# Performance work log

Hardware: AMD Instinct MI355X
Metric: run time of the kernel (lower is better)

## Reference

```python
import jax, jax.numpy as jnp
import numpy as np

N_P, N_A, D_MP = 200000, 100000, 64   # paper nodes, author nodes, metapath embed dim
E = 1200000                            # nnz per adjacency op
F_P, F_A = 256, 128                    # raw feature dims


def _spmm(row, col, val, z, n_out):
    # Sparse [n_out, n_in] @ dense [n_in, d]: out[i] = sum_{e: row[e]==i} val[e] * z[col[e]]
    return jax.ops.segment_sum(val[:, None] * z[col], row, num_segments=n_out)


def setup_inputs() -> dict:
    key = jax.random.key(0)
    k = jax.random.split(key, 10)
    return {
        "x_paper": jax.random.normal(k[0], (N_P, F_P), jnp.float32),
        "x_author": jax.random.normal(k[1], (N_A, F_A), jnp.float32),
        "W_paper": jax.random.normal(k[2], (F_P, D_MP), jnp.float32) / np.float32(np.sqrt(F_P)),
        "W_author": jax.random.normal(k[3], (F_A, D_MP), jnp.float32) / np.float32(np.sqrt(F_A)),
        "pa_row": jax.random.randint(k[4], (E,), 0, N_A, jnp.int32),
        "pa_col": jax.random.randint(k[5], (E,), 0, N_P, jnp.int32),
        "pa_val": jax.random.uniform(k[6], (E,), jnp.float32),
        "ap_row": jax.random.randint(k[7], (E,), 0, N_P, jnp.int32),
        "ap_col": jax.random.randint(k[8], (E,), 0, N_A, jnp.int32),
        "ap_val": jax.random.uniform(k[9], (E,), jnp.float32),
    }


def reference(x_paper, x_author, W_paper, W_author,
              pa_row, pa_col, pa_val, ap_row, ap_col, ap_val):
    # per-node-type projection (nn.Linear, no bias)
    zp = x_paper @ W_paper    # [N_P, D_MP]
    za = x_author @ W_author  # [N_A, D_MP]

    # metapath P-A-P: ops = [pa (N_A x N_P), ap (N_P x N_A)]
    h = _spmm(pa_row, pa_col, pa_val, zp, N_A)
    pap = _spmm(ap_row, ap_col, ap_val, h, N_P)

    # metapath P-A-P-A-P: 4 chained SpMMs
    h2 = _spmm(pa_row, pa_col, pa_val, pap, N_A)
    papap = _spmm(ap_row, ap_col, ap_val, h2, N_P)

    # metapath A-P-A: ops = [ap (N_P x N_A), pa (N_A x N_P)]
    g = _spmm(ap_row, ap_col, ap_val, za, N_P)
    apa = _spmm(pa_row, pa_col, pa_val, g, N_A)

    return (pap, papap, apa)
```

## Files before the change

kernel.cpp:

```cpp
#include <hip/hip_runtime.h>
#include <hip/hip_fp16.h>

#define NP 200000
#define NA 100000
#define NE 1200000


__global__ __launch_bounds__(256) void hist_k(const int* __restrict__ row, int* __restrict__ cnt, int n) {
    int i = blockIdx.x * blockDim.x + threadIdx.x;
    int stride = gridDim.x * blockDim.x;
    for (; i < n; i += stride) atomicAdd(&cnt[row[i]], 1);
}

__global__ __launch_bounds__(256) void scan1_k(const int* __restrict__ in, int* __restrict__ out,
                                               int* __restrict__ bsums, int n) {
    __shared__ int lds[256];
    int t = threadIdx.x;
    int base = blockIdx.x * 1024 + t * 4;
    int v0 = (base + 0 < n) ? in[base + 0] : 0;
    int v1 = (base + 1 < n) ? in[base + 1] : 0;
    int v2 = (base + 2 < n) ? in[base + 2] : 0;
    int v3 = (base + 3 < n) ? in[base + 3] : 0;
    lds[t] = v0 + v1 + v2 + v3;
    __syncthreads();
    for (int off = 1; off < 256; off <<= 1) {
        int x = (t >= off) ? lds[t - off] : 0;
        __syncthreads();
        lds[t] += x;
        __syncthreads();
    }
    if (t == 255) bsums[blockIdx.x] = lds[255];
    int run = (t == 0) ? 0 : lds[t - 1];
    if (base + 0 < n) out[base + 0] = run; run += v0;
    if (base + 1 < n) out[base + 1] = run; run += v1;
    if (base + 2 < n) out[base + 2] = run; run += v2;
    if (base + 3 < n) out[base + 3] = run;
}

__global__ void scan2_k(int* bsums, int nb) {
    __shared__ int lds[256];
    int t = threadIdx.x;
    int v = (t < nb) ? bsums[t] : 0;
    lds[t] = v;
    __syncthreads();
    for (int off = 1; off < 256; off <<= 1) {
        int x = (t >= off) ? lds[t - off] : 0;
        __syncthreads();
        lds[t] += x;
        __syncthreads();
    }
    if (t < nb) bsums[t] = (t == 0) ? 0 : lds[t - 1];
}

__global__ __launch_bounds__(256) void scan3_k(int* __restrict__ out, const int* __restrict__ bsums, int n) {
    int add = bsums[blockIdx.x];
    int base = blockIdx.x * 1024 + threadIdx.x * 4;
#pragma unroll
    for (int j = 0; j < 4; j++)
        if (base + j < n) out[base + j] += add;
}

__global__ __launch_bounds__(256) void scatter_k(const int* __restrict__ row, const int* __restrict__ col,
                                                 const float* __restrict__ val, const int* __restrict__ off,
                                                 int* __restrict__ cursor, int2* __restrict__ csr, int n) {
    int i = blockIdx.x * blockDim.x + threadIdx.x;
    int stride = gridDim.x * blockDim.x;
    for (; i < n; i += stride) {
        int r = row[i];
        int pos = off[r] + atomicAdd(&cursor[r], 1);
        csr[pos] = make_int2(col[i], __float_as_int(val[i]));
    }
}


__device__ __forceinline__ void fma_h8(float acc[8], float v, uint4 r) {
    __half2 h0 = *(__half2*)&r.x;
    __half2 h1 = *(__half2*)&r.y;
    __half2 h2 = *(__half2*)&r.z;
    __half2 h3 = *(__half2*)&r.w;
    float2 f0 = __half22float2(h0);
    float2 f1 = __half22float2(h1);
    float2 f2 = __half22float2(h2);
    float2 f3 = __half22float2(h3);
    acc[0] = fmaf(v, f0.x, acc[0]);
    acc[1] = fmaf(v, f0.y, acc[1]);
    acc[2] = fmaf(v, f1.x, acc[2]);
    acc[3] = fmaf(v, f1.y, acc[3]);
    acc[4] = fmaf(v, f2.x, acc[4]);
    acc[5] = fmaf(v, f2.y, acc[5]);
    acc[6] = fmaf(v, f3.x, acc[6]);
    acc[7] = fmaf(v, f3.y, acc[7]);
}

__device__ __forceinline__ void store_h8(uint4* out16, int g, int l, const float acc[8]) {
    __half2 p0 = __floats2half2_rn(acc[0], acc[1]);
    __half2 p1 = __floats2half2_rn(acc[2], acc[3]);
    __half2 p2 = __floats2half2_rn(acc[4], acc[5]);
    __half2 p3 = __floats2half2_rn(acc[6], acc[7]);
    uint4 o;
    o.x = *(unsigned*)&p0;
    o.y = *(unsigned*)&p1;
    o.z = *(unsigned*)&p2;
    o.w = *(unsigned*)&p3;
    out16[(size_t)g * 8 + l] = o;
}

__device__ __forceinline__ void store_f8(float4* out32, int g, int l, const float acc[8]) {
    out32[(size_t)g * 16 + l * 2 + 0] = make_float4(acc[0], acc[1], acc[2], acc[3]);
    out32[(size_t)g * 16 + l * 2 + 1] = make_float4(acc[4], acc[5], acc[6], acc[7]);
}

__global__ __launch_bounds__(256) void spmm_k(const int2* __restrict__ csr, const int* __restrict__ off,
                                              const int* __restrict__ cnt, const uint4* __restrict__ z,
                                              float4* __restrict__ out32, uint4* __restrict__ out16,
                                              int nrows) {
    int g = blockIdx.x * 32 + (threadIdx.x >> 3);
    int l = threadIdx.x & 7;
    if (g >= nrows) return;
    int start = off[g], deg = cnt[g];
    float acc[8];
#pragma unroll
    for (int i = 0; i < 8; i++) acc[i] = 0.f;
    for (int j = 0; j < deg; j += 4) {
        int j1 = min(j + 1, deg - 1);
        int j2 = min(j + 2, deg - 1);
        int j3 = min(j + 3, deg - 1);
        int2 e0 = csr[start + j];
        int2 e1 = csr[start + j1];
        int2 e2 = csr[start + j2];
        int2 e3 = csr[start + j3];
        uint4 r0 = z[e0.x * 8 + l];
        uint4 r1 = z[e1.x * 8 + l];
        uint4 r2 = z[e2.x * 8 + l];
        uint4 r3 = z[e3.x * 8 + l];
        float v0 = __int_as_float(e0.y);
        float v1 = (j + 1 < deg) ? __int_as_float(e1.y) : 0.f;
        float v2 = (j + 2 < deg) ? __int_as_float(e2.y) : 0.f;
        float v3 = (j + 3 < deg) ? __int_as_float(e3.y) : 0.f;
        fma_h8(acc, v0, r0);
        fma_h8(acc, v1, r1);
        fma_h8(acc, v2, r2);
        fma_h8(acc, v3, r3);
    }
    if (out32) store_f8(out32, g, l, acc);
    if (out16) store_h8(out16, g, l, acc);
}

__global__ __launch_bounds__(256) void spmm2_k(const int2* __restrict__ csr, const int* __restrict__ off,
                                               const int* __restrict__ cnt,
                                               const uint4* __restrict__ zA, const uint4* __restrict__ zB,
                                               float4* __restrict__ outA32, uint4* __restrict__ outA16,
                                               float4* __restrict__ outB32, uint4* __restrict__ outB16,
                                               int nrows) {
    int g = blockIdx.x * 32 + (threadIdx.x >> 3);
    int l = threadIdx.x & 7;
    if (g >= nrows) return;
    int start = off[g], deg = cnt[g];
    float accA[8], accB[8];
#pragma unroll
    for (int i = 0; i < 8; i++) { accA[i] = 0.f; accB[i] = 0.f; }
    for (int j = 0; j < deg; j += 4) {
        int j1 = min(j + 1, deg - 1);
        int j2 = min(j + 2, deg - 1);
        int j3 = min(j + 3, deg - 1);
        int2 e0 = csr[start + j];
        int2 e1 = csr[start + j1];
        int2 e2 = csr[start + j2];
        int2 e3 = csr[start + j3];
        int i0 = e0.x * 8 + l;
        int i1 = e1.x * 8 + l;
        int i2 = e2.x * 8 + l;
        int i3 = e3.x * 8 + l;
        uint4 a0 = zA[i0];
        uint4 a1 = zA[i1];
        uint4 a2 = zA[i2];
        uint4 a3 = zA[i3];
        uint4 b0 = zB[i0];
        uint4 b1 = zB[i1];
        uint4 b2 = zB[i2];
        uint4 b3 = zB[i3];
        float v0 = __int_as_float(e0.y);
        float v1 = (j + 1 < deg) ? __int_as_float(e1.y) : 0.f;
        float v2 = (j + 2 < deg) ? __int_as_float(e2.y) : 0.f;
        float v3 = (j + 3 < deg) ? __int_as_float(e3.y) : 0.f;
        fma_h8(accA, v0, a0);
        fma_h8(accA, v1, a1);
        fma_h8(accA, v2, a2);
        fma_h8(accA, v3, a3);
        fma_h8(accB, v0, b0);
        fma_h8(accB, v1, b1);
        fma_h8(accB, v2, b2);
        fma_h8(accB, v3, b3);
    }
    if (outA32) store_f8(outA32, g, l, accA);
    if (outA16) store_h8(outA16, g, l, accA);
    if (outB32) store_f8(outB32, g, l, accB);
    if (outB16) store_h8(outB16, g, l, accB);
}


template <int K>
__global__ __launch_bounds__(256) void gemm64_k(const float* __restrict__ x, const float* __restrict__ w,
                                                __half* __restrict__ z16, int nrows) {
    __shared__ float xs[32][256];
    __shared__ float wsh[32][64];
    int t = threadIdx.x;
    int tx = t & 7;
    int ty = t >> 3;
    int r0 = blockIdx.x * 256;

    float acc[8][8];
#pragma unroll
    for (int i = 0; i < 8; i++)
#pragma unroll
        for (int j = 0; j < 8; j++) acc[i][j] = 0.f;

    for (int k0 = 0; k0 < K; k0 += 32) {
        __syncthreads();
        {
            int row = r0 + t;
            float4 f[8];
            if (row < nrows) {
                const float* xp = x + (size_t)row * K + k0;
#pragma unroll
                for (int q = 0; q < 8; q++) f[q] = *(const float4*)&xp[q * 4];
            } else {
#pragma unroll
                for (int q = 0; q < 8; q++) f[q] = make_float4(0.f, 0.f, 0.f, 0.f);
            }
#pragma unroll
            for (int q = 0; q < 8; q++) {
                xs[q * 4 + 0][t] = f[q].x;
                xs[q * 4 + 1][t] = f[q].y;
                xs[q * 4 + 2][t] = f[q].z;
                xs[q * 4 + 3][t] = f[q].w;
            }
            const float* wp = w + (size_t)k0 * 64;
            float* wflat = &wsh[0][0];
            *(float4*)&wflat[t * 8 + 0] = *(const float4*)&wp[t * 8 + 0];
            *(float4*)&wflat[t * 8 + 4] = *(const float4*)&wp[t * 8 + 4];
        }
        __syncthreads();
#pragma unroll 8
        for (int kk = 0; kk < 32; kk++) {
            float a[8], b[8];
            *(float4*)&a[0] = *(float4*)&xs[kk][ty * 8 + 0];
            *(float4*)&a[4] = *(float4*)&xs[kk][ty * 8 + 4];
            *(float4*)&b[0] = *(float4*)&wsh[kk][tx * 8 + 0];
            *(float4*)&b[4] = *(float4*)&wsh[kk][tx * 8 + 4];
#pragma unroll
            for (int i = 0; i < 8; i++)
#pragma unroll
                for (int j = 0; j < 8; j++) acc[i][j] = fmaf(a[i], b[j], acc[i][j]);
        }
    }

    int row0 = r0 + ty * 8;
    if (row0 < nrows) {
#pragma unroll
        for (int i = 0; i < 8; i++) {
            __half2 p0 = __floats2half2_rn(acc[i][0], acc[i][1]);
            __half2 p1 = __floats2half2_rn(acc[i][2], acc[i][3]);
            __half2 p2 = __floats2half2_rn(acc[i][4], acc[i][5]);
            __half2 p3 = __floats2half2_rn(acc[i][6], acc[i][7]);
            uint4 o;
            o.x = *(unsigned*)&p0;
            o.y = *(unsigned*)&p1;
            o.z = *(unsigned*)&p2;
            o.w = *(unsigned*)&p3;
            *(uint4*)&z16[(size_t)(row0 + i) * 64 + tx * 8] = o;
        }
    }
}


extern "C" void kernel_launch(void* const* d_in, const int* in_sizes, int n_in,
                              void* d_out, int out_size, void* d_ws, size_t ws_size,
                              hipStream_t stream) {
    const float* x_paper  = (const float*)d_in[0];
    const float* x_author = (const float*)d_in[1];
    const float* W_paper  = (const float*)d_in[2];
    const float* W_author = (const float*)d_in[3];
    const int*   pa_row   = (const int*)d_in[4];
    const int*   pa_col   = (const int*)d_in[5];
    const float* pa_val   = (const float*)d_in[6];
    const int*   ap_row   = (const int*)d_in[7];
    const int*   ap_col   = (const int*)d_in[8];
    const float* ap_val   = (const float*)d_in[9];

    char* ws = (char*)d_ws;
    size_t o = 0;
    auto alloc = [&](size_t bytes) -> char* {
        char* p = ws + o;
        o += (bytes + 255) & ~(size_t)255;
        return p;
    };
    __half* zp16  = (__half*)alloc((size_t)NP * 64 * 2);
    __half* za16  = (__half*)alloc((size_t)NA * 64 * 2);
    __half* h16   = (__half*)alloc((size_t)NA * 64 * 2);
    __half* pap16 = (__half*)alloc((size_t)NP * 64 * 2);
    int2*  csr_pa = (int2*)alloc((size_t)NE * 8);
    int2*  csr_ap = (int2*)alloc((size_t)NE * 8);
    int* cnt_pa = (int*)alloc(NA * 4);
    int* off_pa = (int*)alloc(NA * 4);
    int* cnt_ap = (int*)alloc(NP * 4);
    int* off_ap = (int*)alloc(NP * 4);
    int* cursor = (int*)alloc(NP * 4);
    int* bsums  = (int*)alloc(1024 * 4);

    float* out_pap   = (float*)d_out;
    float* out_papap = out_pap + (size_t)NP * 64;
    float* out_apa   = out_papap + (size_t)NP * 64;

    const int nb_a = (NA + 1023) / 1024;
    const int nb_p = (NP + 1023) / 1024;

    hipMemsetAsync(cnt_pa, 0, NA * 4, stream);
    hipMemsetAsync(cnt_ap, 0, NP * 4, stream);
    hist_k<<<1024, 256, 0, stream>>>(pa_row, cnt_pa, NE);
    hist_k<<<1024, 256, 0, stream>>>(ap_row, cnt_ap, NE);

    scan1_k<<<nb_a, 256, 0, stream>>>(cnt_pa, off_pa, bsums, NA);
    scan2_k<<<1, 256, 0, stream>>>(bsums, nb_a);
    scan3_k<<<nb_a, 256, 0, stream>>>(off_pa, bsums, NA);
    hipMemsetAsync(cursor, 0, NA * 4, stream);
    scatter_k<<<1024, 256, 0, stream>>>(pa_row, pa_col, pa_val, off_pa, cursor, csr_pa, NE);

    scan1_k<<<nb_p, 256, 0, stream>>>(cnt_ap, off_ap, bsums, NP);
    scan2_k<<<1, 256, 0, stream>>>(bsums, nb_p);
    scan3_k<<<nb_p, 256, 0, stream>>>(off_ap, bsums, NP);
    hipMemsetAsync(cursor, 0, NP * 4, stream);
    scatter_k<<<1024, 256, 0, stream>>>(ap_row, ap_col, ap_val, off_ap, cursor, csr_ap, NE);

    gemm64_k<256><<<(NP + 255) / 256, 256, 0, stream>>>(x_paper, W_paper, zp16, NP);
    gemm64_k<128><<<(NA + 255) / 256, 256, 0, stream>>>(x_author, W_author, za16, NA);

    spmm_k<<<NA / 32, 256, 0, stream>>>(csr_pa, off_pa, cnt_pa, (const uint4*)zp16,
                                        nullptr, (uint4*)h16, NA);
    spmm2_k<<<NP / 32, 256, 0, stream>>>(csr_ap, off_ap, cnt_ap,
                                         (const uint4*)h16, (const uint4*)za16,
                                         (float4*)out_pap, (uint4*)pap16,
                                         nullptr, (uint4*)zp16, NP);
    spmm2_k<<<NA / 32, 256, 0, stream>>>(csr_pa, off_pa, cnt_pa,
                                         (const uint4*)pap16, (const uint4*)zp16,
                                         nullptr, (uint4*)h16,
                                         (float4*)out_apa, nullptr, NA);
    spmm_k<<<NP / 32, 256, 0, stream>>>(csr_ap, off_ap, cnt_ap, (const uint4*)h16,
                                        (float4*)out_papap, nullptr, NP);
}
```

Before: 840.4 us.

## Sort rows by degree with a counting sort to balance SpMM wavefronts

Adds a degree histogram, a scan and a scatter that build a permutation of rows grouped by nonzero count for each adjacency. The SpMM kernels process rows through this permutation, so the 8-lane groups sharing a wavefront have similar degrees and less divergence in loop trip count. The cost is six extra small kernels plus memsets, an extra indirection per row, and output writes that become scattered rather than contiguous. With uniformly random row indices the degrees follow a Poisson distribution around 6 or 12, so imbalance is modest.

```diff
diff --git a/kernel.cpp b/kernel.cpp
--- a/kernel.cpp
+++ b/kernel.cpp
@@ -4,6 +4,7 @@
 #define NP 200000
 #define NA 100000
 #define NE 1200000
+#define DBINS 512
 
 
 __global__ __launch_bounds__(256) void hist_k(const int* __restrict__ row, int* __restrict__ cnt, int n) {
@@ -69,6 +70,39 @@
         int r = row[i];
         int pos = off[r] + atomicAdd(&cursor[r], 1);
         csr[pos] = make_int2(col[i], __float_as_int(val[i]));
+    }
+}
+
+
+__global__ __launch_bounds__(256) void dhist_k(const int* __restrict__ cnt, int* __restrict__ dh, int n) {
+    int i = blockIdx.x * blockDim.x + threadIdx.x;
+    int stride = gridDim.x * blockDim.x;
+    for (; i < n; i += stride) atomicAdd(&dh[min(cnt[i], DBINS - 1)], 1);
+}
+
+__global__ void dscan_k(int* dh) {
+    __shared__ int lds[DBINS];
+    int t = threadIdx.x;
+    int v = dh[t];
+    lds[t] = v;
+    __syncthreads();
+    for (int off = 1; off < DBINS; off <<= 1) {
+        int x = (t >= off) ? lds[t - off] : 0;
+        __syncthreads();
+        lds[t] += x;
+        __syncthreads();
+    }
+    dh[t] = lds[t] - v;
+}
+
+__global__ __launch_bounds__(256) void dscatter_k(const int* __restrict__ cnt, const int* __restrict__ doff,
+                                                  int* __restrict__ dcur, int* __restrict__ perm, int n) {
+    int i = blockIdx.x * blockDim.x + threadIdx.x;
+    int stride = gridDim.x * blockDim.x;
+    for (; i < n; i += stride) {
+        int d = min(cnt[i], DBINS - 1);
+        int pos = doff[d] + atomicAdd(&dcur[d], 1);
+        perm[pos] = i;
     }
 }
 
@@ -111,12 +145,14 @@
 }
 
 __global__ __launch_bounds__(256) void spmm_k(const int2* __restrict__ csr, const int* __restrict__ off,
-                                              const int* __restrict__ cnt, const uint4* __restrict__ z,
+                                              const int* __restrict__ cnt, const int* __restrict__ perm,
+                                              const uint4* __restrict__ z,
                                               float4* __restrict__ out32, uint4* __restrict__ out16,
                                               int nrows) {
-    int g = blockIdx.x * 32 + (threadIdx.x >> 3);
+    int gs = blockIdx.x * 32 + (threadIdx.x >> 3);
     int l = threadIdx.x & 7;
-    if (g >= nrows) return;
+    if (gs >= nrows) return;
+    int g = perm[gs];
     int start = off[g], deg = cnt[g];
     float acc[8];
 #pragma unroll
@@ -147,14 +183,15 @@
 }
 
 __global__ __launch_bounds__(256) void spmm2_k(const int2* __restrict__ csr, const int* __restrict__ off,
-                                               const int* __restrict__ cnt,
+                                               const int* __restrict__ cnt, const int* __restrict__ perm,
                                                const uint4* __restrict__ zA, const uint4* __restrict__ zB,
                                                float4* __restrict__ outA32, uint4* __restrict__ outA16,
                                                float4* __restrict__ outB32, uint4* __restrict__ outB16,
                                                int nrows) {
-    int g = blockIdx.x * 32 + (threadIdx.x >> 3);
+    int gs = blockIdx.x * 32 + (threadIdx.x >> 3);
     int l = threadIdx.x & 7;
-    if (g >= nrows) return;
+    if (gs >= nrows) return;
+    int g = perm[gs];
     int start = off[g], deg = cnt[g];
     float accA[8], accB[8];
 #pragma unroll
@@ -305,8 +342,12 @@
     int* off_pa = (int*)alloc(NA * 4);
     int* cnt_ap = (int*)alloc(NP * 4);
     int* off_ap = (int*)alloc(NP * 4);
-    int* cursor = (int*)alloc(NP * 4);
-    int* bsums  = (int*)alloc(1024 * 4);
+    int* cursor  = (int*)alloc(NP * 4);
+    int* bsums   = (int*)alloc(1024 * 4);
+    int* perm_pa = (int*)alloc(NA * 4);
+    int* perm_ap = (int*)alloc(NP * 4);
+    int* dh      = (int*)alloc(DBINS * 4);
+    int* dcur    = (int*)alloc(DBINS * 4);
 
     float* out_pap   = (float*)d_out;
     float* out_papap = out_pap + (size_t)NP * 64;
@@ -332,19 +373,31 @@
     hipMemsetAsync(cursor, 0, NP * 4, stream);
     scatter_k<<<1024, 256, 0, stream>>>(ap_row, ap_col, ap_val, off_ap, cursor, csr_ap, NE);
 
+    hipMemsetAsync(dh, 0, DBINS * 4, stream);
+    dhist_k<<<256, 256, 0, stream>>>(cnt_pa, dh, NA);
+    dscan_k<<<1, DBINS, 0, stream>>>(dh);
+    hipMemsetAsync(dcur, 0, DBINS * 4, stream);
+    dscatter_k<<<256, 256, 0, stream>>>(cnt_pa, dh, dcur, perm_pa, NA);
+
+    hipMemsetAsync(dh, 0, DBINS * 4, stream);
+    dhist_k<<<256, 256, 0, stream>>>(cnt_ap, dh, NP);
+    dscan_k<<<1, DBINS, 0, stream>>>(dh);
+    hipMemsetAsync(dcur, 0, DBINS * 4, stream);
+    dscatter_k<<<256, 256, 0, stream>>>(cnt_ap, dh, dcur, perm_ap, NP);
+
     gemm64_k<256><<<(NP + 255) / 256, 256, 0, stream>>>(x_paper, W_paper, zp16, NP);
     gemm64_k<128><<<(NA + 255) / 256, 256, 0, stream>>>(x_author, W_author, za16, NA);
 
-    spmm_k<<<NA / 32, 256, 0, stream>>>(csr_pa, off_pa, cnt_pa, (const uint4*)zp16,
+    spmm_k<<<NA / 32, 256, 0, stream>>>(csr_pa, off_pa, cnt_pa, perm_pa, (const uint4*)zp16,
                                         nullptr, (uint4*)h16, NA);
-    spmm2_k<<<NP / 32, 256, 0, stream>>>(csr_ap, off_ap, cnt_ap,
+    spmm2_k<<<NP / 32, 256, 0, stream>>>(csr_ap, off_ap, cnt_ap, perm_ap,
                                          (const uint4*)h16, (const uint4*)za16,
                                          (float4*)out_pap, (uint4*)pap16,
                                          nullptr, (uint4*)zp16, NP);
-    spmm2_k<<<NA / 32, 256, 0, stream>>>(csr_pa, off_pa, cnt_pa,
+    spmm2_k<<<NA / 32, 256, 0, stream>>>(csr_pa, off_pa, cnt_pa, perm_pa,
                                          (const uint4*)pap16, (const uint4*)zp16,
                                          nullptr, (uint4*)h16,
                                          (float4*)out_apa, nullptr, NA);
-    spmm_k<<<NP / 32, 256, 0, stream>>>(csr_ap, off_ap, cnt_ap, (const uint4*)h16,
+    spmm_k<<<NP / 32, 256, 0, stream>>>(csr_ap, off_ap, cnt_ap, perm_ap, (const uint4*)h16,
                                         (float4*)out_papap, nullptr, NP);
 }
```

New measurement: 2.962 ms. 3.52x slower.
